# Kernel optimization log

Measured on AMD Instinct MI355X. Metric: run time of the kernel, lower is better.

Reference implementation:

```python
import jax, jax.numpy as jnp
import numpy as np

DIM = 96        # N_VOX/2^(n_scales-layer) = 384/4 at finest layer
C = 24          # ch_in[2]
N_CUR = 150_000
N_GLB = 300_000
N_TGT = 100_000
N_GTGT = 200_000


def setup_inputs() -> dict:
    key = jax.random.key(0)
    ks = jax.random.split(key, 10)
    current_coords = jax.random.randint(ks[0], (N_CUR, 3), 0, DIM, dtype=jnp.int32)
    current_values = jax.random.normal(ks[1], (N_CUR, C), dtype=jnp.float32)
    # global coords live in the global frame; after subtracting the origin some fall outside [0, DIM)
    global_coords = jax.random.randint(ks[2], (N_GLB, 3), 0, DIM + 14, dtype=jnp.int32)
    global_value = jax.random.normal(ks[3], (N_GLB, C), dtype=jnp.float32)
    coords_target_global = jax.random.randint(ks[4], (N_TGT, 3), 0, DIM, dtype=jnp.int32)
    tsdf_target = jax.random.uniform(ks[5], (N_TGT,), minval=-1.0, maxval=1.0, dtype=jnp.float32)
    global_coords_target = jax.random.randint(ks[6], (N_GTGT, 3), 0, DIM + 14, dtype=jnp.int32)
    global_tsdf_target = jax.random.uniform(ks[7], (N_GTGT, 1), minval=-1.0, maxval=1.0, dtype=jnp.float32)
    relative_origin = jnp.array([5, 5, 5], dtype=jnp.int32)
    grid_mask = jax.random.randint(ks[8], (N_CUR,), 0, 2) > 0
    occupancy = jax.random.randint(ks[9], (N_CUR,), 0, 2) > 0
    return dict(current_coords=current_coords, current_values=current_values,
                global_coords=global_coords, global_value=global_value,
                coords_target_global=coords_target_global, tsdf_target=tsdf_target,
                global_coords_target=global_coords_target, global_tsdf_target=global_tsdf_target,
                relative_origin=relative_origin, grid_mask=grid_mask, occupancy=occupancy)


def _masked_idx(coords, mask, dim):
    # rows with mask==False get an out-of-range index -> dropped by scatter mode='drop'
    return jnp.where(mask[:, None], coords, dim)


def reference(current_coords, current_values, global_coords, global_value,
              coords_target_global, tsdf_target, global_coords_target,
              global_tsdf_target, relative_origin, grid_mask, occupancy):
    dim = DIM
    dtype = current_values.dtype
    c = current_values.shape[-1]

    # ---- shift global coords into local fragment frame; in-bounds test ----
    gc = global_coords - relative_origin                       # (Ng, 3)
    in_bounds = jnp.logical_and(gc >= 0, gc < dim).all(-1)     # (Ng,)

    # ---- valid_volume: True where a current voxel inside the camera frusta exists ----
    vi = _masked_idx(current_coords, grid_mask, dim)
    valid_volume = jnp.zeros((dim, dim, dim), dtype=bool).at[vi[:, 0], vi[:, 1], vi[:, 2]].set(True, mode='drop')

    # gather visibility at (clamped) global coords; out-of-bounds rows masked off
    gcc = jnp.clip(gc, 0, dim - 1)
    valid = in_bounds & valid_volume[gcc[:, 0], gcc[:, 1], gcc[:, 2]]   # == local_visible

    # ---- sparse -> dense feature volumes (feat_init = 0) ----
    gi = _masked_idx(gc, valid, dim)
    global_volume = jnp.zeros((dim, dim, dim, c), dtype=dtype).at[gi[:, 0], gi[:, 1], gi[:, 2]].set(global_value, mode='drop')
    cc = current_coords
    current_volume = jnp.zeros((dim, dim, dim, c), dtype=dtype).at[cc[:, 0], cc[:, 1], cc[:, 2]].set(current_values, mode='drop')

    # ---- occupancy volume & updated coordinate mask (dense mask == nonzero set) ----
    oi = _masked_idx(current_coords, occupancy, dim)
    occ_volume = jnp.zeros((dim, dim, dim), dtype=bool).at[oi[:, 0], oi[:, 1], oi[:, 2]].set(True, mode='drop')
    updated_mask = (global_volume != 0).any(-1) | occ_volume

    # voxels in FBV but not visible in current fragment (near set)
    near_mask = in_bounds & jnp.logical_not(valid)

    # ---- ground-truth TSDF fusion (default value = 1) ----
    gct = global_coords_target - relative_origin
    valid_target = jnp.logical_and(gct >= 0, gct < dim).all(-1)
    ti = _masked_idx(gct, valid_target, dim)
    target_volume = jnp.full((dim, dim, dim, 1), 1.0, dtype=dtype)
    target_volume = target_volume.at[ti[:, 0], ti[:, 1], ti[:, 2]].set(global_tsdf_target, mode='drop')
    ct = coords_target_global
    target_volume = target_volume.at[ct[:, 0], ct[:, 1], ct[:, 2]].set(tsdf_target[:, None], mode='drop')

    return (updated_mask, current_volume, global_volume, target_volume, valid, valid_target, near_mask)
```

## Files before the change

### kernel.cpp

```cpp
#include <hip/hip_runtime.h>

#define DIMV 96
#define CCH 24
#define NVOX (DIMV * DIMV * DIMV)
#define QV (NVOX / 4)
#define WORDS (NVOX / 32)
#define ZERO_INTS (2 * WORDS)
#define TOTAL_INTS (ZERO_INTS + 3 * NVOX)
#define N4 (TOTAL_INTS / 4)
#define NZERO4 (ZERO_INTS / 4)

typedef float v4f __attribute__((ext_vector_type(4)));
typedef int   v4i __attribute__((ext_vector_type(4)));

__global__ void init_detect_kernel(v4i* __restrict__ ws_vec,
                                   const unsigned int* __restrict__ mask_words,
                                   int* __restrict__ mode_p) {
    int i = blockIdx.x * blockDim.x + threadIdx.x;
    if (i < N4) {
        int fill = (i < NZERO4) ? 0 : -1;
        v4i val = {fill, fill, fill, fill};
        ws_vec[i] = val;
    }
    if (blockIdx.x == 0) {
        __shared__ int s_byte, s_int, s_float;
        if (threadIdx.x == 0) { s_byte = 0; s_int = 0; s_float = 0; }
        __syncthreads();
        int flag = 0;
        for (int k = 0; k < 4; ++k) {
            unsigned int w = mask_words[threadIdx.x * 4 + k];
            if (w != 0u) {
                if (w == 1u)               flag |= 1;
                else if (w == 0x3F800000u) flag |= 2;
                else                       flag |= 4;
            }
        }
        if (flag & 1) atomicOr(&s_int, 1);
        if (flag & 2) atomicOr(&s_float, 1);
        if (flag & 4) atomicOr(&s_byte, 1);
        __syncthreads();
        if (threadIdx.x == 0)
            *mode_p = s_byte ? 0 : (s_float ? 2 : 1);
    }
}

__device__ __forceinline__ bool read_mask(const void* p, int i, int mode) {
    if (mode == 0) return ((const unsigned char*)p)[i] != 0;
    if (mode == 1) return ((const int*)p)[i] != 0;
    return ((const float*)p)[i] != 0.0f;
}

__global__ void scatter_cur_tgt_kernel(const int* __restrict__ coords,
                                       const void* __restrict__ grid_mask,
                                       const void* __restrict__ occupancy,
                                       const int* __restrict__ mode_p,
                                       unsigned int* __restrict__ valid_bits,
                                       unsigned int* __restrict__ occ_bits,
                                       int* __restrict__ cur_key,
                                       const int* __restrict__ gt_coords,
                                       const int* __restrict__ ct_coords,
                                       const int* __restrict__ origin,
                                       int* __restrict__ tgt_key,
                                       float* __restrict__ out_valid_target,
                                       int n_cur, int n_gtgt, int n_tgt) {
    int i = blockIdx.x * blockDim.x + threadIdx.x;
    if (i < n_cur) {
        int mode = *mode_p;
        int x = coords[3 * i], y = coords[3 * i + 1], z = coords[3 * i + 2];
        if ((unsigned)x >= DIMV || (unsigned)y >= DIMV || (unsigned)z >= DIMV) return;
        int v = (x * DIMV + y) * DIMV + z;
        if (read_mask(grid_mask, i, mode)) atomicOr(&valid_bits[v >> 5], 1u << (v & 31));
        if (read_mask(occupancy, i, mode)) atomicOr(&occ_bits[v >> 5], 1u << (v & 31));
        atomicMax(&cur_key[v], i);
        return;
    }
    int j = i - n_cur;
    if (j < n_gtgt) {
        int x = gt_coords[3 * j] - origin[0];
        int y = gt_coords[3 * j + 1] - origin[1];
        int z = gt_coords[3 * j + 2] - origin[2];
        bool inb = (unsigned)x < DIMV && (unsigned)y < DIMV && (unsigned)z < DIMV;
        out_valid_target[j] = inb ? 1.0f : 0.0f;
        if (inb) atomicMax(&tgt_key[(x * DIMV + y) * DIMV + z], j);
        return;
    }
    int k = j - n_gtgt;
    if (k < n_tgt) {
        int x = ct_coords[3 * k], y = ct_coords[3 * k + 1], z = ct_coords[3 * k + 2];
        if ((unsigned)x < DIMV && (unsigned)y < DIMV && (unsigned)z < DIMV)
            atomicMax(&tgt_key[(x * DIMV + y) * DIMV + z], n_gtgt + k);
    }
}

__global__ void scatter_global_kernel(const int* __restrict__ gcoords,
                                      const int* __restrict__ origin,
                                      const unsigned int* __restrict__ valid_bits,
                                      int* __restrict__ glb_key,
                                      float* __restrict__ out_valid,
                                      float* __restrict__ out_near,
                                      int n) {
    int i = blockIdx.x * blockDim.x + threadIdx.x;
    if (i >= n) return;
    int x = gcoords[3 * i]     - origin[0];
    int y = gcoords[3 * i + 1] - origin[1];
    int z = gcoords[3 * i + 2] - origin[2];
    bool inb = (unsigned)x < DIMV && (unsigned)y < DIMV && (unsigned)z < DIMV;
    bool valid = false;
    if (inb) {
        int v = (x * DIMV + y) * DIMV + z;
        valid = (valid_bits[v >> 5] >> (v & 31)) & 1u;
        if (valid) atomicMax(&glb_key[v], i);
    }
    out_valid[i] = valid ? 1.0f : 0.0f;
    out_near[i]  = (inb && !valid) ? 1.0f : 0.0f;
}

__global__ void resolve_kernel(const v4f* __restrict__ cur_vals4,
                               const v4f* __restrict__ glb_vals4,
                               const float* __restrict__ tsdf_tgt,
                               const float* __restrict__ g_tsdf_tgt,
                               const int* __restrict__ cur_key,
                               const int* __restrict__ glb_key,
                               const int* __restrict__ tgt_key,
                               const unsigned int* __restrict__ occ_bits,
                               float* __restrict__ out_mask,
                               v4f* __restrict__ out_cur4,
                               v4f* __restrict__ out_glb4,
                               float* __restrict__ out_tgt,
                               int n_gtgt) {
    int idx = blockIdx.x * blockDim.x + threadIdx.x;
    int vg = idx / 6;
    int c4 = idx - vg * 6;

    int v[4], ck[4], gk[4];
#pragma unroll
    for (int k = 0; k < 4; ++k) v[k] = vg + k * QV;
#pragma unroll
    for (int k = 0; k < 4; ++k) ck[k] = cur_key[v[k]];
#pragma unroll
    for (int k = 0; k < 4; ++k) gk[k] = glb_key[v[k]];

    v4f z = {0.f, 0.f, 0.f, 0.f};
    v4f a[4], b[4];
#pragma unroll
    for (int k = 0; k < 4; ++k) a[k] = (ck[k] >= 0) ? cur_vals4[ck[k] * 6 + c4] : z;
#pragma unroll
    for (int k = 0; k < 4; ++k) b[k] = (gk[k] >= 0) ? glb_vals4[gk[k] * 6 + c4] : z;

#pragma unroll
    for (int k = 0; k < 4; ++k) __builtin_nontemporal_store(a[k], &out_cur4[v[k] * 6 + c4]);
#pragma unroll
    for (int k = 0; k < 4; ++k) __builtin_nontemporal_store(b[k], &out_glb4[v[k] * 6 + c4]);

    if (c4 == 0) {
#pragma unroll
        for (int k = 0; k < 4; ++k) {
            bool occ = (occ_bits[v[k] >> 5] >> (v[k] & 31)) & 1u;
            out_mask[v[k]] = (gk[k] >= 0 || occ) ? 1.0f : 0.0f;
            int tk = tgt_key[v[k]];
            out_tgt[v[k]] = (tk < 0) ? 1.0f
                          : (tk >= n_gtgt ? tsdf_tgt[tk - n_gtgt] : g_tsdf_tgt[tk]);
        }
    }
}

extern "C" void kernel_launch(void* const* d_in, const int* in_sizes, int n_in,
                              void* d_out, int out_size, void* d_ws, size_t ws_size,
                              hipStream_t stream) {
    const int*   current_coords  = (const int*)  d_in[0];
    const float* current_values  = (const float*)d_in[1];
    const int*   global_coords   = (const int*)  d_in[2];
    const float* global_value    = (const float*)d_in[3];
    const int*   coords_target   = (const int*)  d_in[4];
    const float* tsdf_target     = (const float*)d_in[5];
    const int*   g_coords_target = (const int*)  d_in[6];
    const float* g_tsdf_target   = (const float*)d_in[7];
    const int*   origin          = (const int*)  d_in[8];
    const void*  grid_mask       = d_in[9];
    const void*  occupancy       = d_in[10];

    const int n_cur  = in_sizes[0] / 3;
    const int n_glb  = in_sizes[2] / 3;
    const int n_tgt  = in_sizes[4] / 3;
    const int n_gtgt = in_sizes[6] / 3;

    unsigned int* valid_bits = (unsigned int*)d_ws;
    unsigned int* occ_bits   = valid_bits + WORDS;
    int*          cur_key    = (int*)(occ_bits + WORDS);
    int*          glb_key    = cur_key + NVOX;
    int*          tgt_key    = glb_key + NVOX;
    int*          mode_p     = tgt_key + NVOX;

    float* out     = (float*)d_out;
    float* o_mask  = out;
    float* o_cur   = o_mask + NVOX;
    float* o_glb   = o_cur + NVOX * CCH;
    float* o_tgt   = o_glb + NVOX * CCH;
    float* o_valid = o_tgt + NVOX;
    float* o_vtgt  = o_valid + n_glb;
    float* o_near  = o_vtgt + n_gtgt;

    init_detect_kernel<<<(N4 + 255) / 256, 256, 0, stream>>>(
        (v4i*)d_ws, (const unsigned int*)grid_mask, mode_p);

    scatter_cur_tgt_kernel<<<(n_cur + n_gtgt + n_tgt + 255) / 256, 256, 0, stream>>>(
        current_coords, grid_mask, occupancy, mode_p, valid_bits, occ_bits, cur_key,
        g_coords_target, coords_target, origin, tgt_key, o_vtgt,
        n_cur, n_gtgt, n_tgt);

    scatter_global_kernel<<<(n_glb + 255) / 256, 256, 0, stream>>>(
        global_coords, origin, valid_bits, glb_key, o_valid, o_near, n_glb);

    resolve_kernel<<<(QV * 6) / 256, 256, 0, stream>>>(
        (const v4f*)current_values, (const v4f*)global_value,
        tsdf_target, g_tsdf_target, cur_key, glb_key, tgt_key, occ_bits,
        o_mask, (v4f*)o_cur, (v4f*)o_glb, o_tgt, n_gtgt);
}
```

Baseline: 277.7 us.

## Replace dense resolve pass with bulk fill plus sparse winner-only writes

The dense output volumes are now written by a bulk constant fill: zeros for the mask and feature volumes, ones for the target volume. The fill is fused into the scatter kernel as extra blocks. A new winners kernel then iterates over the input points rather than voxels. Each point writes its feature row only if it won the atomicMax key, and it also sets mask entries directly, which drops the occupancy bitmap. This removes the per-voxel key reads and gathers, but the sparse writes are scattered and non-coalesced, and the fill still streams the full output.

```diff
diff --git a/kernel.cpp b/kernel.cpp
--- a/kernel.cpp
+++ b/kernel.cpp
@@ -3,12 +3,14 @@
 #define DIMV 96
 #define CCH 24
 #define NVOX (DIMV * DIMV * DIMV)
-#define QV (NVOX / 4)
 #define WORDS (NVOX / 32)
-#define ZERO_INTS (2 * WORDS)
-#define TOTAL_INTS (ZERO_INTS + 3 * NVOX)
-#define N4 (TOTAL_INTS / 4)
-#define NZERO4 (ZERO_INTS / 4)
+#define TOTAL_INTS (WORDS + 3 * NVOX)
+#define N4I (TOTAL_INTS / 4)
+#define NZERO4 (WORDS / 4)
+
+#define FILL_V4 (NVOX * 50 / 4)
+#define ZV4 (NVOX * 49 / 4)
+#define FILL_BLOCKS (FILL_V4 / 1024)
 
 typedef float v4f __attribute__((ext_vector_type(4)));
 typedef int   v4i __attribute__((ext_vector_type(4)));
@@ -17,7 +19,7 @@
                                    const unsigned int* __restrict__ mask_words,
                                    int* __restrict__ mode_p) {
     int i = blockIdx.x * blockDim.x + threadIdx.x;
-    if (i < N4) {
+    if (i < N4I) {
         int fill = (i < NZERO4) ? 0 : -1;
         v4i val = {fill, fill, fill, fill};
         ws_vec[i] = val;
@@ -50,27 +52,36 @@
     return ((const float*)p)[i] != 0.0f;
 }
 
-__global__ void scatter_cur_tgt_kernel(const int* __restrict__ coords,
-                                       const void* __restrict__ grid_mask,
-                                       const void* __restrict__ occupancy,
-                                       const int* __restrict__ mode_p,
-                                       unsigned int* __restrict__ valid_bits,
-                                       unsigned int* __restrict__ occ_bits,
-                                       int* __restrict__ cur_key,
-                                       const int* __restrict__ gt_coords,
-                                       const int* __restrict__ ct_coords,
-                                       const int* __restrict__ origin,
-                                       int* __restrict__ tgt_key,
-                                       float* __restrict__ out_valid_target,
-                                       int n_cur, int n_gtgt, int n_tgt) {
+__global__ void fill_scatter_kernel(v4f* __restrict__ out_dense,
+                                    const int* __restrict__ coords,
+                                    const void* __restrict__ grid_mask,
+                                    const int* __restrict__ mode_p,
+                                    unsigned int* __restrict__ valid_bits,
+                                    int* __restrict__ cur_key,
+                                    const int* __restrict__ gt_coords,
+                                    const int* __restrict__ ct_coords,
+                                    const int* __restrict__ origin,
+                                    int* __restrict__ tgt_key,
+                                    float* __restrict__ out_valid_target,
+                                    int n_cur, int n_gtgt, int n_tgt, int sb) {
+    if ((int)blockIdx.x >= sb) {
+        int base = (blockIdx.x - sb) * 1024 + threadIdx.x;
+        v4f zero = {0.f, 0.f, 0.f, 0.f};
+        v4f one  = {1.f, 1.f, 1.f, 1.f};
+#pragma unroll
+        for (int k = 0; k < 4; ++k) {
+            int idx = base + k * 256;
+            __builtin_nontemporal_store(idx < ZV4 ? zero : one, &out_dense[idx]);
+        }
+        return;
+    }
     int i = blockIdx.x * blockDim.x + threadIdx.x;
     if (i < n_cur) {
-        int mode = *mode_p;
         int x = coords[3 * i], y = coords[3 * i + 1], z = coords[3 * i + 2];
         if ((unsigned)x >= DIMV || (unsigned)y >= DIMV || (unsigned)z >= DIMV) return;
         int v = (x * DIMV + y) * DIMV + z;
-        if (read_mask(grid_mask, i, mode)) atomicOr(&valid_bits[v >> 5], 1u << (v & 31));
-        if (read_mask(occupancy, i, mode)) atomicOr(&occ_bits[v >> 5], 1u << (v & 31));
+        if (read_mask(grid_mask, i, *mode_p))
+            atomicOr(&valid_bits[v >> 5], 1u << (v & 31));
         atomicMax(&cur_key[v], i);
         return;
     }
@@ -115,51 +126,71 @@
     out_near[i]  = (inb && !valid) ? 1.0f : 0.0f;
 }
 
-__global__ void resolve_kernel(const v4f* __restrict__ cur_vals4,
+__global__ void winners_kernel(const v4f* __restrict__ cur_vals4,
                                const v4f* __restrict__ glb_vals4,
+                               const int* __restrict__ coords,
+                               const int* __restrict__ gcoords,
+                               const int* __restrict__ gt_coords,
+                               const int* __restrict__ ct_coords,
                                const float* __restrict__ tsdf_tgt,
                                const float* __restrict__ g_tsdf_tgt,
+                               const void* __restrict__ occupancy,
+                               const int* __restrict__ mode_p,
+                               const int* __restrict__ origin,
                                const int* __restrict__ cur_key,
                                const int* __restrict__ glb_key,
                                const int* __restrict__ tgt_key,
-                               const unsigned int* __restrict__ occ_bits,
+                               const float* __restrict__ o_valid,
                                float* __restrict__ out_mask,
                                v4f* __restrict__ out_cur4,
                                v4f* __restrict__ out_glb4,
                                float* __restrict__ out_tgt,
-                               int n_gtgt) {
-    int idx = blockIdx.x * blockDim.x + threadIdx.x;
-    int vg = idx / 6;
-    int c4 = idx - vg * 6;
-
-    int v[4], ck[4], gk[4];
+                               int n_cur, int n_glb, int n_gtgt, int n_tgt) {
+    int i = blockIdx.x * blockDim.x + threadIdx.x;
+    if (i < n_cur) {
+        int x = coords[3 * i], y = coords[3 * i + 1], z = coords[3 * i + 2];
+        if ((unsigned)x >= DIMV || (unsigned)y >= DIMV || (unsigned)z >= DIMV) return;
+        int v = (x * DIMV + y) * DIMV + z;
+        if (read_mask(occupancy, i, *mode_p)) out_mask[v] = 1.0f;
+        if (cur_key[v] == i) {
 #pragma unroll
-    for (int k = 0; k < 4; ++k) v[k] = vg + k * QV;
+            for (int c = 0; c < 6; ++c)
+                __builtin_nontemporal_store(cur_vals4[i * 6 + c], &out_cur4[v * 6 + c]);
+        }
+        return;
+    }
+    int j = i - n_cur;
+    if (j < n_glb) {
+        if (o_valid[j] == 0.0f) return;
+        int x = gcoords[3 * j]     - origin[0];
+        int y = gcoords[3 * j + 1] - origin[1];
+        int z = gcoords[3 * j + 2] - origin[2];
+        int v = (x * DIMV + y) * DIMV + z;
+        out_mask[v] = 1.0f;
+        if (glb_key[v] == j) {
 #pragma unroll
-    for (int k = 0; k < 4; ++k) ck[k] = cur_key[v[k]];
-#pragma unroll
-    for (int k = 0; k < 4; ++k) gk[k] = glb_key[v[k]];
-
-    v4f z = {0.f, 0.f, 0.f, 0.f};
-    v4f a[4], b[4];
-#pragma unroll
-    for (int k = 0; k < 4; ++k) a[k] = (ck[k] >= 0) ? cur_vals4[ck[k] * 6 + c4] : z;
-#pragma unroll
-    for (int k = 0; k < 4; ++k) b[k] = (gk[k] >= 0) ? glb_vals4[gk[k] * 6 + c4] : z;
-
-#pragma unroll
-    for (int k = 0; k < 4; ++k) __builtin_nontemporal_store(a[k], &out_cur4[v[k] * 6 + c4]);
-#pragma unroll
-    for (int k = 0; k < 4; ++k) __builtin_nontemporal_store(b[k], &out_glb4[v[k] * 6 + c4]);
-
-    if (c4 == 0) {
-#pragma unroll
-        for (int k = 0; k < 4; ++k) {
-            bool occ = (occ_bits[v[k] >> 5] >> (v[k] & 31)) & 1u;
-            out_mask[v[k]] = (gk[k] >= 0 || occ) ? 1.0f : 0.0f;
-            int tk = tgt_key[v[k]];
-            out_tgt[v[k]] = (tk < 0) ? 1.0f
-                          : (tk >= n_gtgt ? tsdf_tgt[tk - n_gtgt] : g_tsdf_tgt[tk]);
+            for (int c = 0; c < 6; ++c)
+                __builtin_nontemporal_store(glb_vals4[j * 6 + c], &out_glb4[v * 6 + c]);
+        }
+        return;
+    }
+    int t = j - n_glb;
+    if (t < n_gtgt) {
+        int x = gt_coords[3 * t] - origin[0];
+        int y = gt_coords[3 * t + 1] - origin[1];
+        int z = gt_coords[3 * t + 2] - origin[2];
+        if ((unsigned)x < DIMV && (unsigned)y < DIMV && (unsigned)z < DIMV) {
+            int v = (x * DIMV + y) * DIMV + z;
+            if (tgt_key[v] == t) out_tgt[v] = g_tsdf_tgt[t];
+        }
+        return;
+    }
+    int k = t - n_gtgt;
+    if (k < n_tgt) {
+        int x = ct_coords[3 * k], y = ct_coords[3 * k + 1], z = ct_coords[3 * k + 2];
+        if ((unsigned)x < DIMV && (unsigned)y < DIMV && (unsigned)z < DIMV) {
+            int v = (x * DIMV + y) * DIMV + z;
+            if (tgt_key[v] == n_gtgt + k) out_tgt[v] = tsdf_tgt[k];
         }
     }
 }
@@ -185,8 +216,7 @@
     const int n_gtgt = in_sizes[6] / 3;
 
     unsigned int* valid_bits = (unsigned int*)d_ws;
-    unsigned int* occ_bits   = valid_bits + WORDS;
-    int*          cur_key    = (int*)(occ_bits + WORDS);
+    int*          cur_key    = (int*)(valid_bits + WORDS);
     int*          glb_key    = cur_key + NVOX;
     int*          tgt_key    = glb_key + NVOX;
     int*          mode_p     = tgt_key + NVOX;
@@ -200,19 +230,24 @@
     float* o_vtgt  = o_valid + n_glb;
     float* o_near  = o_vtgt + n_gtgt;
 
-    init_detect_kernel<<<(N4 + 255) / 256, 256, 0, stream>>>(
+    init_detect_kernel<<<(N4I + 255) / 256, 256, 0, stream>>>(
         (v4i*)d_ws, (const unsigned int*)grid_mask, mode_p);
 
-    scatter_cur_tgt_kernel<<<(n_cur + n_gtgt + n_tgt + 255) / 256, 256, 0, stream>>>(
-        current_coords, grid_mask, occupancy, mode_p, valid_bits, occ_bits, cur_key,
+    const int sb = (n_cur + n_gtgt + n_tgt + 255) / 256;
+    fill_scatter_kernel<<<sb + FILL_BLOCKS, 256, 0, stream>>>(
+        (v4f*)o_mask,
+        current_coords, grid_mask, mode_p, valid_bits, cur_key,
         g_coords_target, coords_target, origin, tgt_key, o_vtgt,
-        n_cur, n_gtgt, n_tgt);
+        n_cur, n_gtgt, n_tgt, sb);
 
     scatter_global_kernel<<<(n_glb + 255) / 256, 256, 0, stream>>>(
         global_coords, origin, valid_bits, glb_key, o_valid, o_near, n_glb);
 
-    resolve_kernel<<<(QV * 6) / 256, 256, 0, stream>>>(
+    winners_kernel<<<(n_cur + n_glb + n_gtgt + n_tgt + 255) / 256, 256, 0, stream>>>(
         (const v4f*)current_values, (const v4f*)global_value,
-        tsdf_target, g_tsdf_target, cur_key, glb_key, tgt_key, occ_bits,
-        o_mask, (v4f*)o_cur, (v4f*)o_glb, o_tgt, n_gtgt);
-}
+        current_coords, global_coords, g_coords_target, coords_target,
+        tsdf_target, g_tsdf_target, occupancy, mode_p, origin,
+        cur_key, glb_key, tgt_key, o_valid,
+        o_mask, (v4f*)o_cur, (v4f*)o_glb, o_tgt,
+        n_cur, n_glb, n_gtgt, n_tgt);
+}
```

Measured after the change: 309.7 us. 11.5% more time.

## Interleave cur/glb keys and split resolve into payload, mask and target block groups

Applied to the files above, without the earlier changes.

Stores the current and global winner keys interleaved as int2 per voxel, so the payload gather reads both with one 8-byte load. The resolve kernel is split into block ranges: payload blocks handle two voxels per thread with contiguous output indexing, while separate mask and target blocks process four voxels per thread with vector loads and nontemporal float4 stores. This removes the divergent c4==0 branch and the scalar mask/target stores. The trade-off is fewer voxels per payload thread and more blocks in the launch.

```diff
diff --git a/kernel.cpp b/kernel.cpp
--- a/kernel.cpp
+++ b/kernel.cpp
@@ -3,21 +3,27 @@
 #define DIMV 96
 #define CCH 24
 #define NVOX (DIMV * DIMV * DIMV)
-#define QV (NVOX / 4)
+#define HALFV (NVOX / 2)
 #define WORDS (NVOX / 32)
 #define ZERO_INTS (2 * WORDS)
 #define TOTAL_INTS (ZERO_INTS + 3 * NVOX)
-#define N4 (TOTAL_INTS / 4)
+#define N4I (TOTAL_INTS / 4)
 #define NZERO4 (ZERO_INTS / 4)
+
+#define PAYLOAD_BLOCKS (HALFV * 6 / 256)
+#define MASK_BLOCKS (NVOX / 1024)
+#define TGT_BLOCKS (NVOX / 1024)
+#define RESOLVE_BLOCKS (PAYLOAD_BLOCKS + MASK_BLOCKS + TGT_BLOCKS)
 
 typedef float v4f __attribute__((ext_vector_type(4)));
 typedef int   v4i __attribute__((ext_vector_type(4)));
+typedef int   v2i __attribute__((ext_vector_type(2)));
 
 __global__ void init_detect_kernel(v4i* __restrict__ ws_vec,
                                    const unsigned int* __restrict__ mask_words,
                                    int* __restrict__ mode_p) {
     int i = blockIdx.x * blockDim.x + threadIdx.x;
-    if (i < N4) {
+    if (i < N4I) {
         int fill = (i < NZERO4) ? 0 : -1;
         v4i val = {fill, fill, fill, fill};
         ws_vec[i] = val;
@@ -56,7 +62,7 @@
                                        const int* __restrict__ mode_p,
                                        unsigned int* __restrict__ valid_bits,
                                        unsigned int* __restrict__ occ_bits,
-                                       int* __restrict__ cur_key,
+                                       int* __restrict__ key2,
                                        const int* __restrict__ gt_coords,
                                        const int* __restrict__ ct_coords,
                                        const int* __restrict__ origin,
@@ -71,7 +77,7 @@
         int v = (x * DIMV + y) * DIMV + z;
         if (read_mask(grid_mask, i, mode)) atomicOr(&valid_bits[v >> 5], 1u << (v & 31));
         if (read_mask(occupancy, i, mode)) atomicOr(&occ_bits[v >> 5], 1u << (v & 31));
-        atomicMax(&cur_key[v], i);
+        atomicMax(&key2[2 * v], i);
         return;
     }
     int j = i - n_cur;
@@ -95,7 +101,7 @@
 __global__ void scatter_global_kernel(const int* __restrict__ gcoords,
                                       const int* __restrict__ origin,
                                       const unsigned int* __restrict__ valid_bits,
-                                      int* __restrict__ glb_key,
+                                      int* __restrict__ key2,
                                       float* __restrict__ out_valid,
                                       float* __restrict__ out_near,
                                       int n) {
@@ -109,7 +115,7 @@
     if (inb) {
         int v = (x * DIMV + y) * DIMV + z;
         valid = (valid_bits[v >> 5] >> (v & 31)) & 1u;
-        if (valid) atomicMax(&glb_key[v], i);
+        if (valid) atomicMax(&key2[2 * v + 1], i);
     }
     out_valid[i] = valid ? 1.0f : 0.0f;
     out_near[i]  = (inb && !valid) ? 1.0f : 0.0f;
@@ -119,48 +125,60 @@
                                const v4f* __restrict__ glb_vals4,
                                const float* __restrict__ tsdf_tgt,
                                const float* __restrict__ g_tsdf_tgt,
-                               const int* __restrict__ cur_key,
-                               const int* __restrict__ glb_key,
-                               const int* __restrict__ tgt_key,
+                               const v2i* __restrict__ key2_2,
+                               const v4i* __restrict__ key2_4,
+                               const v4i* __restrict__ tgt_key4,
                                const unsigned int* __restrict__ occ_bits,
-                               float* __restrict__ out_mask,
+                               v4f* __restrict__ out_mask4,
                                v4f* __restrict__ out_cur4,
                                v4f* __restrict__ out_glb4,
-                               float* __restrict__ out_tgt,
+                               v4f* __restrict__ out_tgt4,
                                int n_gtgt) {
-    int idx = blockIdx.x * blockDim.x + threadIdx.x;
-    int vg = idx / 6;
-    int c4 = idx - vg * 6;
-
-    int v[4], ck[4], gk[4];
-#pragma unroll
-    for (int k = 0; k < 4; ++k) v[k] = vg + k * QV;
-#pragma unroll
-    for (int k = 0; k < 4; ++k) ck[k] = cur_key[v[k]];
-#pragma unroll
-    for (int k = 0; k < 4; ++k) gk[k] = glb_key[v[k]];
-
-    v4f z = {0.f, 0.f, 0.f, 0.f};
-    v4f a[4], b[4];
-#pragma unroll
-    for (int k = 0; k < 4; ++k) a[k] = (ck[k] >= 0) ? cur_vals4[ck[k] * 6 + c4] : z;
-#pragma unroll
-    for (int k = 0; k < 4; ++k) b[k] = (gk[k] >= 0) ? glb_vals4[gk[k] * 6 + c4] : z;
-
-#pragma unroll
-    for (int k = 0; k < 4; ++k) __builtin_nontemporal_store(a[k], &out_cur4[v[k] * 6 + c4]);
-#pragma unroll
-    for (int k = 0; k < 4; ++k) __builtin_nontemporal_store(b[k], &out_glb4[v[k] * 6 + c4]);
-
-    if (c4 == 0) {
-#pragma unroll
-        for (int k = 0; k < 4; ++k) {
-            bool occ = (occ_bits[v[k] >> 5] >> (v[k] & 31)) & 1u;
-            out_mask[v[k]] = (gk[k] >= 0 || occ) ? 1.0f : 0.0f;
-            int tk = tgt_key[v[k]];
-            out_tgt[v[k]] = (tk < 0) ? 1.0f
-                          : (tk >= n_gtgt ? tsdf_tgt[tk - n_gtgt] : g_tsdf_tgt[tk]);
-        }
+    int b = blockIdx.x;
+    if (b < PAYLOAD_BLOCKS) {
+        int idx = b * 256 + threadIdx.x;
+        int p  = idx / 6;
+        int c4 = idx - p * 6;
+        int v0 = p, v1 = p + HALFV;
+
+        v2i k0 = key2_2[v0];
+        v2i k1 = key2_2[v1];
+
+        v4f z = {0.f, 0.f, 0.f, 0.f};
+        v4f a0 = (k0.x >= 0) ? cur_vals4[k0.x * 6 + c4] : z;
+        v4f a1 = (k1.x >= 0) ? cur_vals4[k1.x * 6 + c4] : z;
+        v4f b0 = (k0.y >= 0) ? glb_vals4[k0.y * 6 + c4] : z;
+        v4f b1 = (k1.y >= 0) ? glb_vals4[k1.y * 6 + c4] : z;
+
+        __builtin_nontemporal_store(a0, &out_cur4[idx]);
+        __builtin_nontemporal_store(a1, &out_cur4[idx + HALFV * 6]);
+        __builtin_nontemporal_store(b0, &out_glb4[idx]);
+        __builtin_nontemporal_store(b1, &out_glb4[idx + HALFV * 6]);
+        return;
+    }
+    if (b < PAYLOAD_BLOCKS + MASK_BLOCKS) {
+        int t = (b - PAYLOAD_BLOCKS) * 256 + threadIdx.x;
+        int v = 4 * t;
+        v4i A = key2_4[2 * t];
+        v4i B = key2_4[2 * t + 1];
+        unsigned int occw = occ_bits[v >> 5] >> (v & 31);
+        v4f m;
+        m.x = (A.y >= 0 || (occw & 1u)) ? 1.0f : 0.0f;
+        m.y = (A.w >= 0 || ((occw >> 1) & 1u)) ? 1.0f : 0.0f;
+        m.z = (B.y >= 0 || ((occw >> 2) & 1u)) ? 1.0f : 0.0f;
+        m.w = (B.w >= 0 || ((occw >> 3) & 1u)) ? 1.0f : 0.0f;
+        __builtin_nontemporal_store(m, &out_mask4[t]);
+        return;
+    }
+    {
+        int t = (b - PAYLOAD_BLOCKS - MASK_BLOCKS) * 256 + threadIdx.x;
+        v4i T = tgt_key4[t];
+        v4f r;
+        r.x = (T.x < 0) ? 1.0f : (T.x >= n_gtgt ? tsdf_tgt[T.x - n_gtgt] : g_tsdf_tgt[T.x]);
+        r.y = (T.y < 0) ? 1.0f : (T.y >= n_gtgt ? tsdf_tgt[T.y - n_gtgt] : g_tsdf_tgt[T.y]);
+        r.z = (T.z < 0) ? 1.0f : (T.z >= n_gtgt ? tsdf_tgt[T.z - n_gtgt] : g_tsdf_tgt[T.z]);
+        r.w = (T.w < 0) ? 1.0f : (T.w >= n_gtgt ? tsdf_tgt[T.w - n_gtgt] : g_tsdf_tgt[T.w]);
+        __builtin_nontemporal_store(r, &out_tgt4[t]);
     }
 }
 
@@ -186,9 +204,8 @@
 
     unsigned int* valid_bits = (unsigned int*)d_ws;
     unsigned int* occ_bits   = valid_bits + WORDS;
-    int*          cur_key    = (int*)(occ_bits + WORDS);
-    int*          glb_key    = cur_key + NVOX;
-    int*          tgt_key    = glb_key + NVOX;
+    int*          key2       = (int*)(occ_bits + WORDS);
+    int*          tgt_key    = key2 + 2 * NVOX;
     int*          mode_p     = tgt_key + NVOX;
 
     float* out     = (float*)d_out;
@@ -200,19 +217,20 @@
     float* o_vtgt  = o_valid + n_glb;
     float* o_near  = o_vtgt + n_gtgt;
 
-    init_detect_kernel<<<(N4 + 255) / 256, 256, 0, stream>>>(
+    init_detect_kernel<<<(N4I + 255) / 256, 256, 0, stream>>>(
         (v4i*)d_ws, (const unsigned int*)grid_mask, mode_p);
 
     scatter_cur_tgt_kernel<<<(n_cur + n_gtgt + n_tgt + 255) / 256, 256, 0, stream>>>(
-        current_coords, grid_mask, occupancy, mode_p, valid_bits, occ_bits, cur_key,
+        current_coords, grid_mask, occupancy, mode_p, valid_bits, occ_bits, key2,
         g_coords_target, coords_target, origin, tgt_key, o_vtgt,
         n_cur, n_gtgt, n_tgt);
 
     scatter_global_kernel<<<(n_glb + 255) / 256, 256, 0, stream>>>(
-        global_coords, origin, valid_bits, glb_key, o_valid, o_near, n_glb);
-
-    resolve_kernel<<<(QV * 6) / 256, 256, 0, stream>>>(
+        global_coords, origin, valid_bits, key2, o_valid, o_near, n_glb);
+
+    resolve_kernel<<<RESOLVE_BLOCKS, 256, 0, stream>>>(
         (const v4f*)current_values, (const v4f*)global_value,
-        tsdf_target, g_tsdf_target, cur_key, glb_key, tgt_key, occ_bits,
-        o_mask, (v4f*)o_cur, (v4f*)o_glb, o_tgt, n_gtgt);
-}
+        tsdf_target, g_tsdf_target,
+        (const v2i*)key2, (const v4i*)key2, (const v4i*)tgt_key, occ_bits,
+        (v4f*)o_mask, (v4f*)o_cur, (v4f*)o_glb, (v4f*)o_tgt, n_gtgt);
+}
```

After: 269.1 us. 1.03x faster.
